# Kernel optimization log

Measured on AMD Instinct MI355X. Metric: run time of the kernel, lower is better.

The kernel has to match this reference:

```python
import jax, jax.numpy as jnp
import numpy as np

IN_C = 256
KEY_C = 256
VAL_C = 256
HEADS = 8


def setup_inputs() -> dict:
    key = jax.random.key(0)
    ks = jax.random.split(key, 9)
    s = 0.02
    return {
        "x": jax.random.normal(ks[0], (4, 8192, IN_C), dtype=jnp.float32),
        "Wk": jax.random.normal(ks[1], (KEY_C, IN_C), dtype=jnp.float32) * s,
        "bk": jax.random.normal(ks[2], (KEY_C,), dtype=jnp.float32) * s,
        "Wq": jax.random.normal(ks[3], (KEY_C, IN_C), dtype=jnp.float32) * s,
        "bq": jax.random.normal(ks[4], (KEY_C,), dtype=jnp.float32) * s,
        "Wv": jax.random.normal(ks[5], (VAL_C, IN_C), dtype=jnp.float32) * s,
        "bv": jax.random.normal(ks[6], (VAL_C,), dtype=jnp.float32) * s,
        "Wr": jax.random.normal(ks[7], (IN_C, VAL_C), dtype=jnp.float32) * s,
        "br": jax.random.normal(ks[8], (IN_C,), dtype=jnp.float32) * s,
    }


def reference(x, Wk, bk, Wq, bq, Wv, bv, Wr, br):
    n, N, c = x.shape
    # Faithful to torch: reshape (NOT transpose) of (n, N, c) into (n, c, N)
    xi = x.reshape(n, c, N)
    # 1x1 convs == channel-mixing matmuls over the token axis
    K = jnp.einsum('oc,ncs->nos', Wk, xi) + bk[None, :, None]
    Q = jnp.einsum('oc,ncs->nos', Wq, xi) + bq[None, :, None]
    V = jnp.einsum('oc,ncs->nos', Wv, xi) + bv[None, :, None]
    dk = KEY_C // HEADS
    dv = VAL_C // HEADS
    Kh = K.reshape(n, HEADS, dk, N)
    Qh = Q.reshape(n, HEADS, dk, N)
    Vh = V.reshape(n, HEADS, dv, N)
    # keys: softmax over tokens (dim=2); queries: softmax over head key channels (dim=1)
    Kh = jax.nn.softmax(Kh, axis=3)
    Qh = jax.nn.softmax(Qh, axis=2)
    # context = K @ V^T : [n, H, dk, dv]
    ctx = jnp.einsum('nhks,nhvs->nhkv', Kh, Vh)
    # attended = context^T @ Q : [n, H, dv, N]
    att = jnp.einsum('nhkv,nhks->nhvs', ctx, Qh)
    agg = att.reshape(n, VAL_C, N)
    rep = jnp.einsum('ov,nvs->nos', Wr, agg) + br[None, :, None]
    out = rep + xi  # residual in (n, c, N) layout
    return jnp.transpose(out, (0, 2, 1))  # (n, N, c)
```

## Files before the change

### kernel.cpp

```cpp
#include <hip/hip_runtime.h>

#define NTOK 8192
#define NCH  256
#define TT   64
#define XTP  264
#define EKP  72

typedef unsigned short u16;
typedef __attribute__((ext_vector_type(8))) short bf16x8;
typedef __attribute__((ext_vector_type(4))) float f32x4;
typedef __attribute__((ext_vector_type(8))) unsigned short u16x8;
typedef __attribute__((ext_vector_type(4))) unsigned short u16x4;

__device__ __forceinline__ float b2f(u16 h){
  union{unsigned u; float f;} x; x.u = ((unsigned)h) << 16; return x.f;
}
__device__ __forceinline__ u16 f2b(float f){
  union{float f; unsigned u;} x; x.f = f;
  unsigned u = x.u;
  return (u16)((u + 0x7FFFu + ((u >> 16) & 1u)) >> 16);
}
__device__ __forceinline__ f32x4 mfma16(bf16x8 a, bf16x8 b, f32x4 c){
  return __builtin_amdgcn_mfma_f32_16x16x32_bf16(a, b, c, 0, 0, 0);
}

__global__ __launch_bounds__(256)
void k_prep(const float* __restrict__ x,
            const float* __restrict__ Wk, const float* __restrict__ Wq,
            const float* __restrict__ Wv, const float* __restrict__ Wr,
            u16* __restrict__ xT, u16* __restrict__ wbf)
{
  __shared__ u16 ts[64 * 68];
  const int t = threadIdx.x, bid = blockIdx.x;
  if (bid < 2048) {
    const int b = bid >> 9, rem = bid & 511, tg = rem >> 2, cg = rem & 3;
    const float* xb = x + (size_t)b * NCH * NTOK;
    #pragma unroll
    for (int p = 0; p < 4; ++p) {
      int cl = p * 16 + (t >> 4);
      int tl = (t & 15) * 4;
      float4 v = *(const float4*)(xb + (size_t)(cg * 64 + cl) * NTOK + tg * 64 + tl);
      u16x4 pk; pk[0]=f2b(v.x); pk[1]=f2b(v.y); pk[2]=f2b(v.z); pk[3]=f2b(v.w);
      *(u16x4*)&ts[cl * 68 + tl] = pk;
    }
    __syncthreads();
    #pragma unroll
    for (int p = 0; p < 2; ++p) {
      int tl = p * 32 + (t >> 3);
      int cl = (t & 7) * 8;
      u16x8 o;
      #pragma unroll
      for (int j = 0; j < 8; ++j) o[j] = ts[(cl + j) * 68 + tl];
      *(u16x8*)(xT + (((size_t)(b * NTOK + tg * 64 + tl)) << 8) + cg * 64 + cl) = o;
    }
  } else {
    const int wb = bid - 2048;
    const int mat = wb >> 4;
    const float* src = (mat == 0) ? Wk : (mat == 1) ? Wq : (mat == 2) ? Wv : Wr;
    u16* dst = wbf + mat * 65536;
    const int base = (wb & 15) * 4096 + t * 16;
    #pragma unroll
    for (int i = 0; i < 4; ++i) {
      float4 v = *(const float4*)(src + base + i * 4);
      u16x4 pk; pk[0]=f2b(v.x); pk[1]=f2b(v.y); pk[2]=f2b(v.z); pk[3]=f2b(v.w);
      *(u16x4*)(dst + base + i * 4) = pk;
    }
  }
}

__global__ __launch_bounds__(512)
void k_ctx(const u16* __restrict__ xT, const u16* __restrict__ wbf,
           const float* __restrict__ bk, const float* __restrict__ bv,
           u16* __restrict__ ctxPart, float* __restrict__ denomPart)
{
  __shared__ u16 bufA[NCH * EKP];
  __shared__ u16 ekb[NCH * EKP];

  const int t = threadIdx.x;
  const int b = blockIdx.x >> 7, g = blockIdx.x & 127;
  const int w = t >> 6, lane = t & 63;
  const int l15 = lane & 15, quad = lane >> 4;
  const u16* Wkb = wbf;
  const u16* Wvb = wbf + 2 * 65536;

  {
    const u16* src = xT + ((size_t)(b * NTOK + g * TT) << 8);
    #pragma unroll
    for (int i = 0; i < 4; ++i) {
      int f = i * 4096 + t * 8;
      int tok = f >> 8, ch = f & 255;
      *(u16x8*)&bufA[tok * XTP + ch] = *(const u16x8*)(src + f);
    }
  }
  __syncthreads();

  f32x4 acc[2][4];

  #pragma unroll
  for (int mi = 0; mi < 2; ++mi)
    #pragma unroll
    for (int nj = 0; nj < 4; ++nj) acc[mi][nj] = (f32x4)0.f;
  for (int k0 = 0; k0 < NCH; k0 += 32) {
    bf16x8 af[2], bx[4];
    #pragma unroll
    for (int mi = 0; mi < 2; ++mi)
      af[mi] = *(const bf16x8*)(Wkb + (size_t)(w * 32 + mi * 16 + l15) * NCH + k0 + quad * 8);
    #pragma unroll
    for (int nj = 0; nj < 4; ++nj)
      bx[nj] = *(const bf16x8*)&bufA[(nj * 16 + l15) * XTP + k0 + quad * 8];
    #pragma unroll
    for (int mi = 0; mi < 2; ++mi)
      #pragma unroll
      for (int nj = 0; nj < 4; ++nj) acc[mi][nj] = mfma16(af[mi], bx[nj], acc[mi][nj]);
  }
  #pragma unroll
  for (int mi = 0; mi < 2; ++mi) {
    float4 bb = *(const float4*)(bk + w * 32 + mi * 16 + quad * 4);
    #pragma unroll
    for (int nj = 0; nj < 4; ++nj) {
      int tok = nj * 16 + l15, chb = w * 32 + mi * 16 + quad * 4;
      ekb[(chb + 0) * EKP + tok] = f2b(__expf(acc[mi][nj][0] + bb.x));
      ekb[(chb + 1) * EKP + tok] = f2b(__expf(acc[mi][nj][1] + bb.y));
      ekb[(chb + 2) * EKP + tok] = f2b(__expf(acc[mi][nj][2] + bb.z));
      ekb[(chb + 3) * EKP + tok] = f2b(__expf(acc[mi][nj][3] + bb.w));
    }
  }

  #pragma unroll
  for (int mi = 0; mi < 2; ++mi)
    #pragma unroll
    for (int nj = 0; nj < 4; ++nj) acc[mi][nj] = (f32x4)0.f;
  for (int k0 = 0; k0 < NCH; k0 += 32) {
    bf16x8 af[2], bx[4];
    #pragma unroll
    for (int mi = 0; mi < 2; ++mi)
      af[mi] = *(const bf16x8*)(Wvb + (size_t)(w * 32 + mi * 16 + l15) * NCH + k0 + quad * 8);
    #pragma unroll
    for (int nj = 0; nj < 4; ++nj)
      bx[nj] = *(const bf16x8*)&bufA[(nj * 16 + l15) * XTP + k0 + quad * 8];
    #pragma unroll
    for (int mi = 0; mi < 2; ++mi)
      #pragma unroll
      for (int nj = 0; nj < 4; ++nj) acc[mi][nj] = mfma16(af[mi], bx[nj], acc[mi][nj]);
  }
  __syncthreads();
  #pragma unroll
  for (int mi = 0; mi < 2; ++mi) {
    float4 bb = *(const float4*)(bv + w * 32 + mi * 16 + quad * 4);
    #pragma unroll
    for (int nj = 0; nj < 4; ++nj) {
      int tok = nj * 16 + l15, chb = w * 32 + mi * 16 + quad * 4;
      bufA[(chb + 0) * EKP + tok] = f2b(acc[mi][nj][0] + bb.x);
      bufA[(chb + 1) * EKP + tok] = f2b(acc[mi][nj][1] + bb.y);
      bufA[(chb + 2) * EKP + tok] = f2b(acc[mi][nj][2] + bb.z);
      bufA[(chb + 3) * EKP + tok] = f2b(acc[mi][nj][3] + bb.w);
    }
  }
  __syncthreads();

  f32x4 cacc[2][2];
  #pragma unroll
  for (int mi = 0; mi < 2; ++mi)
    #pragma unroll
    for (int nj = 0; nj < 2; ++nj) cacc[mi][nj] = (f32x4)0.f;
  #pragma unroll
  for (int kc = 0; kc < 2; ++kc) {
    bf16x8 ae[2], bvv[2];
    #pragma unroll
    for (int mi = 0; mi < 2; ++mi)
      ae[mi] = *(const bf16x8*)&ekb[(w * 32 + mi * 16 + l15) * EKP + kc * 32 + quad * 8];
    #pragma unroll
    for (int nj = 0; nj < 2; ++nj)
      bvv[nj] = *(const bf16x8*)&bufA[(w * 32 + nj * 16 + l15) * EKP + kc * 32 + quad * 8];
    #pragma unroll
    for (int mi = 0; mi < 2; ++mi)
      #pragma unroll
      for (int nj = 0; nj < 2; ++nj)
        cacc[mi][nj] = mfma16(ae[mi], bvv[nj], cacc[mi][nj]);
  }
  float dsum = 0.f;
  if (t < 256) {
    #pragma unroll
    for (int s = 0; s < TT; s += 8) {
      u16x8 v = *(const u16x8*)&ekb[t * EKP + s];
      #pragma unroll
      for (int j = 0; j < 8; ++j) dsum += b2f(v[j]);
    }
  }

  u16* cp = ctxPart + ((size_t)(b * 128 + g) << 13);
  #pragma unroll
  for (int mi = 0; mi < 2; ++mi)
    #pragma unroll
    for (int nj = 0; nj < 2; ++nj)
      #pragma unroll
      for (int r = 0; r < 4; ++r) {
        int e = ((w * 32 + mi * 16 + quad * 4 + r) << 5) + nj * 16 + l15;
        cp[e] = f2b(cacc[mi][nj][r]);
      }
  if (t < 256)
    denomPart[(size_t)(b * 128 + g) * 256 + t] = dsum;
}

__global__ __launch_bounds__(256)
void k_red(const u16* __restrict__ ctxPart, const float* __restrict__ denomPart,
           u16* __restrict__ ctxT, float* __restrict__ rdenomF)
{
  int i = blockIdx.x * 256 + threadIdx.x;
  if (i < 32768) {
    int b = i >> 13, e = i & 8191;
    const u16* p = ctxPart + ((size_t)(b * 128) << 13) + e;
    float s = 0.f;
    for (int g = 0; g < 128; ++g) s += b2f(p[(size_t)g << 13]);
    int hh = e >> 10, kk = (e >> 5) & 31, vch = e & 31;
    ctxT[(((b * 8 + hh) * 32 + vch) << 5) + kk] = f2b(s);
  } else if (i < 33792) {
    int j = i - 32768, b = j >> 8, ch = j & 255;
    const float* p = denomPart + (size_t)(b * 128) * 256 + ch;
    float s = 0.f;
    for (int g = 0; g < 128; ++g) s += p[(size_t)g << 8];
    rdenomF[j] = 1.0f / s;
  }
}

__global__ __launch_bounds__(512)
void k_out(const u16* __restrict__ xT, const u16* __restrict__ wbf,
           const float* __restrict__ bq, const float* __restrict__ br,
           const u16* __restrict__ ctxT, const float* __restrict__ rdenomF,
           float* __restrict__ out)
{
  __shared__ u16 xs[TT * XTP];
  __shared__ u16 qs[TT * XTP];

  const int t = threadIdx.x;
  const int b = blockIdx.x >> 7, g = blockIdx.x & 127;
  const int w = t >> 6, lane = t & 63;
  const int l15 = lane & 15, quad = lane >> 4;
  const u16* Wqb = wbf + 65536;
  const u16* Wrb = wbf + 3 * 65536;

  {
    const u16* src = xT + ((size_t)(b * NTOK + g * TT) << 8);
    #pragma unroll
    for (int i = 0; i < 4; ++i) {
      int f = i * 4096 + t * 8;
      int tok = f >> 8, ch = f & 255;
      *(u16x8*)&xs[tok * XTP + ch] = *(const u16x8*)(src + f);
    }
  }
  __syncthreads();

  f32x4 acc[2][4];
  #pragma unroll
  for (int mi = 0; mi < 2; ++mi)
    #pragma unroll
    for (int nj = 0; nj < 4; ++nj) acc[mi][nj] = (f32x4)0.f;
  for (int k0 = 0; k0 < NCH; k0 += 32) {
    bf16x8 af[2], bx[4];
    #pragma unroll
    for (int mi = 0; mi < 2; ++mi)
      af[mi] = *(const bf16x8*)(Wqb + (size_t)(w * 32 + mi * 16 + l15) * NCH + k0 + quad * 8);
    #pragma unroll
    for (int nj = 0; nj < 4; ++nj)
      bx[nj] = *(const bf16x8*)&xs[(nj * 16 + l15) * XTP + k0 + quad * 8];
    #pragma unroll
    for (int mi = 0; mi < 2; ++mi)
      #pragma unroll
      for (int nj = 0; nj < 4; ++nj) acc[mi][nj] = mfma16(af[mi], bx[nj], acc[mi][nj]);
  }
  #pragma unroll
  for (int mi = 0; mi < 2; ++mi) {
    float4 bb = *(const float4*)(bq + w * 32 + mi * 16 + quad * 4);
    #pragma unroll
    for (int nj = 0; nj < 4; ++nj) {
      acc[mi][nj][0] = __expf(acc[mi][nj][0] + bb.x);
      acc[mi][nj][1] = __expf(acc[mi][nj][1] + bb.y);
      acc[mi][nj][2] = __expf(acc[mi][nj][2] + bb.z);
      acc[mi][nj][3] = __expf(acc[mi][nj][3] + bb.w);
    }
  }
  float inv[4];
  #pragma unroll
  for (int nj = 0; nj < 4; ++nj) {
    float s = 0.f;
    #pragma unroll
    for (int mi = 0; mi < 2; ++mi)
      #pragma unroll
      for (int r = 0; r < 4; ++r) s += acc[mi][nj][r];
    s += __shfl_xor(s, 16);
    s += __shfl_xor(s, 32);
    inv[nj] = 1.0f / s;
  }
  #pragma unroll
  for (int mi = 0; mi < 2; ++mi) {
    float4 rd = *(const float4*)(rdenomF + b * 256 + w * 32 + mi * 16 + quad * 4);
    #pragma unroll
    for (int nj = 0; nj < 4; ++nj) {
      u16x4 pk;
      pk[0] = f2b(acc[mi][nj][0] * inv[nj] * rd.x);
      pk[1] = f2b(acc[mi][nj][1] * inv[nj] * rd.y);
      pk[2] = f2b(acc[mi][nj][2] * inv[nj] * rd.z);
      pk[3] = f2b(acc[mi][nj][3] * inv[nj] * rd.w);
      *(u16x4*)&qs[(nj * 16 + l15) * XTP + w * 32 + mi * 16 + quad * 4] = pk;
    }
  }
  __syncthreads();

  f32x4 aacc[2][4];
  {
    bf16x8 ac[2];
    #pragma unroll
    for (int mi = 0; mi < 2; ++mi)
      ac[mi] = *(const bf16x8*)(ctxT + (((size_t)(b * 8 + w) * 32 + mi * 16 + l15) << 5) + quad * 8);
    #pragma unroll
    for (int nj = 0; nj < 4; ++nj) {
      bf16x8 bqf = *(const bf16x8*)&qs[(nj * 16 + l15) * XTP + w * 32 + quad * 8];
      #pragma unroll
      for (int mi = 0; mi < 2; ++mi)
        aacc[mi][nj] = mfma16(ac[mi], bqf, (f32x4)0.f);
    }
  }
  #pragma unroll
  for (int mi = 0; mi < 2; ++mi)
    #pragma unroll
    for (int nj = 0; nj < 4; ++nj) {
      u16x4 pk;
      pk[0] = f2b(aacc[mi][nj][0]);
      pk[1] = f2b(aacc[mi][nj][1]);
      pk[2] = f2b(aacc[mi][nj][2]);
      pk[3] = f2b(aacc[mi][nj][3]);
      *(u16x4*)&qs[(nj * 16 + l15) * XTP + w * 32 + mi * 16 + quad * 4] = pk;
    }
  __syncthreads();

  #pragma unroll
  for (int mi = 0; mi < 2; ++mi)
    #pragma unroll
    for (int nj = 0; nj < 4; ++nj) acc[mi][nj] = (f32x4)0.f;
  for (int k0 = 0; k0 < NCH; k0 += 32) {
    bf16x8 af[2], bx[4];
    #pragma unroll
    for (int mi = 0; mi < 2; ++mi)
      af[mi] = *(const bf16x8*)(Wrb + (size_t)(w * 32 + mi * 16 + l15) * NCH + k0 + quad * 8);
    #pragma unroll
    for (int nj = 0; nj < 4; ++nj)
      bx[nj] = *(const bf16x8*)&qs[(nj * 16 + l15) * XTP + k0 + quad * 8];
    #pragma unroll
    for (int mi = 0; mi < 2; ++mi)
      #pragma unroll
      for (int nj = 0; nj < 4; ++nj) acc[mi][nj] = mfma16(af[mi], bx[nj], acc[mi][nj]);
  }
  #pragma unroll
  for (int mi = 0; mi < 2; ++mi) {
    float4 bb = *(const float4*)(br + w * 32 + mi * 16 + quad * 4);
    #pragma unroll
    for (int nj = 0; nj < 4; ++nj) {
      int tok = nj * 16 + l15;
      u16x4 rx = *(const u16x4*)&xs[tok * XTP + w * 32 + mi * 16 + quad * 4];
      float4 o;
      o.x = acc[mi][nj][0] + bb.x + b2f(rx[0]);
      o.y = acc[mi][nj][1] + bb.y + b2f(rx[1]);
      o.z = acc[mi][nj][2] + bb.z + b2f(rx[2]);
      o.w = acc[mi][nj][3] + bb.w + b2f(rx[3]);
      *(float4*)(out + (((size_t)(b * NTOK + g * TT + tok)) << 8) + w * 32 + mi * 16 + quad * 4) = o;
    }
  }
}

extern "C" void kernel_launch(void* const* d_in, const int* in_sizes, int n_in,
                              void* d_out, int out_size, void* d_ws, size_t ws_size,
                              hipStream_t stream) {
  const float* x  = (const float*)d_in[0];
  const float* Wk = (const float*)d_in[1];
  const float* bk = (const float*)d_in[2];
  const float* Wq = (const float*)d_in[3];
  const float* bq = (const float*)d_in[4];
  const float* Wv = (const float*)d_in[5];
  const float* bv = (const float*)d_in[6];
  const float* Wr = (const float*)d_in[7];
  const float* br = (const float*)d_in[8];
  float* out = (float*)d_out;

  char* wsb = (char*)d_ws;
  u16*   ctxPart   = (u16*)wsb;
  float* denomPart = (float*)(wsb + 8388608);
  u16*   ctxT      = (u16*)(wsb + 8912896);
  float* rdenomF   = (float*)(wsb + 8978432);
  u16*   wbf       = (u16*)(wsb + 8982528);
  u16*   xT        = (u16*)(wsb + 9506816);

  hipLaunchKernelGGL(k_prep, dim3(2112), dim3(256), 0, stream,
                     x, Wk, Wq, Wv, Wr, xT, wbf);
  hipLaunchKernelGGL(k_ctx, dim3(512), dim3(512), 0, stream,
                     xT, wbf, bk, bv, ctxPart, denomPart);
  hipLaunchKernelGGL(k_red, dim3(132), dim3(256), 0, stream,
                     ctxPart, denomPart, ctxT, rdenomF);
  hipLaunchKernelGGL(k_out, dim3(512), dim3(512), 0, stream,
                     xT, wbf, bq, br, ctxT, rdenomF, out);
}
```

Before: 148.5 us.

## Fuse prep, context, reduction and output kernels into one cooperative grid-synced kernel

Replaces the four launches with a single cooperative kernel of 256 blocks that each handle two token tiles, separated by grid.sync barriers. The x transpose and bf16 conversion now happen in shared memory inside the fused kernel, and the bf16 x tile is stored for reuse in the output phase. Weight fragments are held in registers across the k loop, and the partial reduction runs over 64 parts instead of 128. This removes launch gaps and some global round trips, at the cost of grid-wide syncs and only 256 blocks, which may leave compute units underused.

```diff
diff --git a/kernel.cpp b/kernel.cpp
--- a/kernel.cpp
+++ b/kernel.cpp
@@ -1,10 +1,14 @@
 #include <hip/hip_runtime.h>
+#include <hip/hip_cooperative_groups.h>
+
+namespace cg = cooperative_groups;
 
 #define NTOK 8192
 #define NCH  256
 #define TT   64
 #define XTP  264
 #define EKP  72
+#define TAP  70
 
 typedef unsigned short u16;
 typedef __attribute__((ext_vector_type(8))) short bf16x8;
@@ -23,347 +27,370 @@
 __device__ __forceinline__ f32x4 mfma16(bf16x8 a, bf16x8 b, f32x4 c){
   return __builtin_amdgcn_mfma_f32_16x16x32_bf16(a, b, c, 0, 0, 0);
 }
-
-__global__ __launch_bounds__(256)
-void k_prep(const float* __restrict__ x,
-            const float* __restrict__ Wk, const float* __restrict__ Wq,
-            const float* __restrict__ Wv, const float* __restrict__ Wr,
-            u16* __restrict__ xT, u16* __restrict__ wbf)
+__device__ __forceinline__ void load_wfrags(const u16* __restrict__ Wb, int row,
+                                            int quad, bf16x8* wf){
+  const u16* p = Wb + (size_t)row * NCH + quad * 8;
+  #pragma unroll
+  for (int k = 0; k < 8; ++k) wf[k] = *(const bf16x8*)(p + k * 32);
+}
+
+__global__ __launch_bounds__(512, 4)
+void k_fused(const float* __restrict__ x,
+             const float* __restrict__ Wk, const float* __restrict__ Wq,
+             const float* __restrict__ Wv, const float* __restrict__ Wr,
+             const float* __restrict__ bk, const float* __restrict__ bq,
+             const float* __restrict__ bv, const float* __restrict__ br,
+             u16* __restrict__ wbf, u16* __restrict__ xT,
+             u16* __restrict__ ctxPart, float* __restrict__ denomPart,
+             u16* __restrict__ ctxT, float* __restrict__ rdenomF,
+             float* __restrict__ out)
 {
-  __shared__ u16 ts[64 * 68];
-  const int t = threadIdx.x, bid = blockIdx.x;
-  if (bid < 2048) {
-    const int b = bid >> 9, rem = bid & 511, tg = rem >> 2, cg = rem & 3;
-    const float* xb = x + (size_t)b * NCH * NTOK;
-    #pragma unroll
-    for (int p = 0; p < 4; ++p) {
-      int cl = p * 16 + (t >> 4);
-      int tl = (t & 15) * 4;
-      float4 v = *(const float4*)(xb + (size_t)(cg * 64 + cl) * NTOK + tg * 64 + tl);
-      u16x4 pk; pk[0]=f2b(v.x); pk[1]=f2b(v.y); pk[2]=f2b(v.z); pk[3]=f2b(v.w);
-      *(u16x4*)&ts[cl * 68 + tl] = pk;
-    }
-    __syncthreads();
-    #pragma unroll
-    for (int p = 0; p < 2; ++p) {
-      int tl = p * 32 + (t >> 3);
-      int cl = (t & 7) * 8;
-      u16x8 o;
-      #pragma unroll
-      for (int j = 0; j < 8; ++j) o[j] = ts[(cl + j) * 68 + tl];
-      *(u16x8*)(xT + (((size_t)(b * NTOK + tg * 64 + tl)) << 8) + cg * 64 + cl) = o;
-    }
-  } else {
-    const int wb = bid - 2048;
-    const int mat = wb >> 4;
+  __shared__ u16 reg1[NCH * EKP];
+  __shared__ u16 reg2[NCH * EKP];
+
+  cg::grid_group grid = cg::this_grid();
+
+  const int t = threadIdx.x;
+  const int bid = blockIdx.x;
+  const int b = bid >> 6;
+  const int g0 = (bid & 63) * 2;
+  const int w = t >> 6, lane = t & 63;
+  const int l15 = lane & 15, quad = lane >> 4;
+  const int tok_t = t & 63, chb = (t >> 6) * 32;
+
+  if (bid < 64) {
+    const int mat = bid >> 4;
     const float* src = (mat == 0) ? Wk : (mat == 1) ? Wq : (mat == 2) ? Wv : Wr;
     u16* dst = wbf + mat * 65536;
-    const int base = (wb & 15) * 4096 + t * 16;
-    #pragma unroll
-    for (int i = 0; i < 4; ++i) {
+    const int base = (bid & 15) * 4096 + t * 8;
+    #pragma unroll
+    for (int i = 0; i < 2; ++i) {
       float4 v = *(const float4*)(src + base + i * 4);
       u16x4 pk; pk[0]=f2b(v.x); pk[1]=f2b(v.y); pk[2]=f2b(v.z); pk[3]=f2b(v.w);
       *(u16x4*)(dst + base + i * 4) = pk;
     }
-  }
-}
-
-__global__ __launch_bounds__(512)
-void k_ctx(const u16* __restrict__ xT, const u16* __restrict__ wbf,
-           const float* __restrict__ bk, const float* __restrict__ bv,
-           u16* __restrict__ ctxPart, float* __restrict__ denomPart)
-{
-  __shared__ u16 bufA[NCH * EKP];
-  __shared__ u16 ekb[NCH * EKP];
-
-  const int t = threadIdx.x;
-  const int b = blockIdx.x >> 7, g = blockIdx.x & 127;
-  const int w = t >> 6, lane = t & 63;
-  const int l15 = lane & 15, quad = lane >> 4;
-  const u16* Wkb = wbf;
-  const u16* Wvb = wbf + 2 * 65536;
+    __threadfence();
+  }
 
   {
-    const u16* src = xT + ((size_t)(b * NTOK + g * TT) << 8);
-    #pragma unroll
-    for (int i = 0; i < 4; ++i) {
-      int f = i * 4096 + t * 8;
-      int tok = f >> 8, ch = f & 255;
-      *(u16x8*)&bufA[tok * XTP + ch] = *(const u16x8*)(src + f);
-    }
-  }
-  __syncthreads();
-
-  f32x4 acc[2][4];
-
-  #pragma unroll
-  for (int mi = 0; mi < 2; ++mi)
-    #pragma unroll
-    for (int nj = 0; nj < 4; ++nj) acc[mi][nj] = (f32x4)0.f;
-  for (int k0 = 0; k0 < NCH; k0 += 32) {
-    bf16x8 af[2], bx[4];
-    #pragma unroll
-    for (int mi = 0; mi < 2; ++mi)
-      af[mi] = *(const bf16x8*)(Wkb + (size_t)(w * 32 + mi * 16 + l15) * NCH + k0 + quad * 8);
-    #pragma unroll
-    for (int nj = 0; nj < 4; ++nj)
-      bx[nj] = *(const bf16x8*)&bufA[(nj * 16 + l15) * XTP + k0 + quad * 8];
-    #pragma unroll
-    for (int mi = 0; mi < 2; ++mi)
-      #pragma unroll
-      for (int nj = 0; nj < 4; ++nj) acc[mi][nj] = mfma16(af[mi], bx[nj], acc[mi][nj]);
-  }
-  #pragma unroll
-  for (int mi = 0; mi < 2; ++mi) {
-    float4 bb = *(const float4*)(bk + w * 32 + mi * 16 + quad * 4);
-    #pragma unroll
-    for (int nj = 0; nj < 4; ++nj) {
-      int tok = nj * 16 + l15, chb = w * 32 + mi * 16 + quad * 4;
-      ekb[(chb + 0) * EKP + tok] = f2b(__expf(acc[mi][nj][0] + bb.x));
-      ekb[(chb + 1) * EKP + tok] = f2b(__expf(acc[mi][nj][1] + bb.y));
-      ekb[(chb + 2) * EKP + tok] = f2b(__expf(acc[mi][nj][2] + bb.z));
-      ekb[(chb + 3) * EKP + tok] = f2b(__expf(acc[mi][nj][3] + bb.w));
-    }
-  }
-
-  #pragma unroll
-  for (int mi = 0; mi < 2; ++mi)
-    #pragma unroll
-    for (int nj = 0; nj < 4; ++nj) acc[mi][nj] = (f32x4)0.f;
-  for (int k0 = 0; k0 < NCH; k0 += 32) {
-    bf16x8 af[2], bx[4];
-    #pragma unroll
-    for (int mi = 0; mi < 2; ++mi)
-      af[mi] = *(const bf16x8*)(Wvb + (size_t)(w * 32 + mi * 16 + l15) * NCH + k0 + quad * 8);
-    #pragma unroll
-    for (int nj = 0; nj < 4; ++nj)
-      bx[nj] = *(const bf16x8*)&bufA[(nj * 16 + l15) * XTP + k0 + quad * 8];
-    #pragma unroll
-    for (int mi = 0; mi < 2; ++mi)
-      #pragma unroll
-      for (int nj = 0; nj < 4; ++nj) acc[mi][nj] = mfma16(af[mi], bx[nj], acc[mi][nj]);
+    const float* xb = x + ((size_t)b * NCH) * NTOK + g0 * TT;
+    const int tq = (t & 15) * 4, ch0 = t >> 4;
+    #pragma unroll
+    for (int p = 0; p < 8; ++p) {
+      int ch = p * 32 + ch0;
+      float4 v = *(const float4*)(xb + (size_t)ch * NTOK + tq);
+      u16x4 pk; pk[0]=f2b(v.x); pk[1]=f2b(v.y); pk[2]=f2b(v.z); pk[3]=f2b(v.w);
+      *(u16x4*)&reg2[ch * TAP + tq] = pk;
+    }
   }
   __syncthreads();
   #pragma unroll
-  for (int mi = 0; mi < 2; ++mi) {
-    float4 bb = *(const float4*)(bv + w * 32 + mi * 16 + quad * 4);
-    #pragma unroll
-    for (int nj = 0; nj < 4; ++nj) {
-      int tok = nj * 16 + l15, chb = w * 32 + mi * 16 + quad * 4;
-      bufA[(chb + 0) * EKP + tok] = f2b(acc[mi][nj][0] + bb.x);
-      bufA[(chb + 1) * EKP + tok] = f2b(acc[mi][nj][1] + bb.y);
-      bufA[(chb + 2) * EKP + tok] = f2b(acc[mi][nj][2] + bb.z);
-      bufA[(chb + 3) * EKP + tok] = f2b(acc[mi][nj][3] + bb.w);
-    }
-  }
-  __syncthreads();
+  for (int i = 0; i < 4; ++i) {
+    u16x8 v;
+    #pragma unroll
+    for (int j = 0; j < 8; ++j) v[j] = reg2[(chb + i * 8 + j) * TAP + tok_t];
+    *(u16x8*)&reg1[tok_t * XTP + chb + i * 8] = v;
+  }
+  grid.sync();
+
+  const u16* Wkb = wbf;
+  const u16* Wqb = wbf + 65536;
+  const u16* Wvb = wbf + 2 * 65536;
+  const u16* Wrb = wbf + 3 * 65536;
 
   f32x4 cacc[2][2];
   #pragma unroll
   for (int mi = 0; mi < 2; ++mi)
     #pragma unroll
     for (int nj = 0; nj < 2; ++nj) cacc[mi][nj] = (f32x4)0.f;
-  #pragma unroll
-  for (int kc = 0; kc < 2; ++kc) {
-    bf16x8 ae[2], bvv[2];
+  float dsum = 0.f;
+
+  for (int c = 0; c < 2; ++c) {
+    if (c == 1) {
+      const float* xb = x + ((size_t)b * NCH) * NTOK + (g0 + 1) * TT;
+      const int tq = (t & 15) * 4, ch0 = t >> 4;
+      #pragma unroll
+      for (int p = 0; p < 8; ++p) {
+        int ch = p * 32 + ch0;
+        float4 v = *(const float4*)(xb + (size_t)ch * NTOK + tq);
+        u16x4 pk; pk[0]=f2b(v.x); pk[1]=f2b(v.y); pk[2]=f2b(v.z); pk[3]=f2b(v.w);
+        *(u16x4*)&reg2[ch * TAP + tq] = pk;
+      }
+      __syncthreads();
+      #pragma unroll
+      for (int i = 0; i < 4; ++i) {
+        u16x8 v;
+        #pragma unroll
+        for (int j = 0; j < 8; ++j) v[j] = reg2[(chb + i * 8 + j) * TAP + tok_t];
+        *(u16x8*)&reg1[tok_t * XTP + chb + i * 8] = v;
+      }
+      __syncthreads();
+    }
+
+    bf16x8 wfA[8], wfB[8];
+    load_wfrags(Wkb, w * 32 + l15, quad, wfA);
+
+    {
+      u16* dst = xT + ((size_t)(bid * 2 + c)) * 16384;
+      #pragma unroll
+      for (int i = 0; i < 4; ++i) {
+        int f = i * 4096 + t * 8;
+        *(u16x8*)(dst + f) = *(const u16x8*)&reg1[(f >> 8) * XTP + (f & 255)];
+      }
+    }
+
+    const u16* abase = &reg1[l15 * XTP + quad * 8];
+    f32x4 acc0[4], acc1[4];
+
+    load_wfrags(Wkb, w * 32 + 16 + l15, quad, wfB);
+    #pragma unroll
+    for (int mi = 0; mi < 4; ++mi) acc0[mi] = (f32x4)0.f;
+    #pragma unroll
+    for (int k = 0; k < 8; ++k) {
+      #pragma unroll
+      for (int mi = 0; mi < 4; ++mi) {
+        bf16x8 a = *(const bf16x8*)(abase + mi * 16 * XTP + k * 32);
+        acc0[mi] = mfma16(a, wfA[k], acc0[mi]);
+      }
+    }
+    {
+      float bb = bk[w * 32 + l15];
+      #pragma unroll
+      for (int mi = 0; mi < 4; ++mi) {
+        u16x4 pk;
+        #pragma unroll
+        for (int r = 0; r < 4; ++r) pk[r] = f2b(__expf(acc0[mi][r] + bb));
+        *(u16x4*)&reg2[(w * 32 + l15) * EKP + mi * 16 + quad * 4] = pk;
+      }
+    }
+    load_wfrags(Wvb, w * 32 + l15, quad, wfA);
+    #pragma unroll
+    for (int mi = 0; mi < 4; ++mi) acc0[mi] = (f32x4)0.f;
+    #pragma unroll
+    for (int k = 0; k < 8; ++k) {
+      #pragma unroll
+      for (int mi = 0; mi < 4; ++mi) {
+        bf16x8 a = *(const bf16x8*)(abase + mi * 16 * XTP + k * 32);
+        acc0[mi] = mfma16(a, wfB[k], acc0[mi]);
+      }
+    }
+    {
+      float bb = bk[w * 32 + 16 + l15];
+      #pragma unroll
+      for (int mi = 0; mi < 4; ++mi) {
+        u16x4 pk;
+        #pragma unroll
+        for (int r = 0; r < 4; ++r) pk[r] = f2b(__expf(acc0[mi][r] + bb));
+        *(u16x4*)&reg2[(w * 32 + 16 + l15) * EKP + mi * 16 + quad * 4] = pk;
+      }
+    }
+    load_wfrags(Wvb, w * 32 + 16 + l15, quad, wfB);
+    #pragma unroll
+    for (int mi = 0; mi < 4; ++mi) { acc0[mi] = (f32x4)0.f; acc1[mi] = (f32x4)0.f; }
+    #pragma unroll
+    for (int k = 0; k < 8; ++k) {
+      #pragma unroll
+      for (int mi = 0; mi < 4; ++mi) {
+        bf16x8 a = *(const bf16x8*)(abase + mi * 16 * XTP + k * 32);
+        acc0[mi] = mfma16(a, wfA[k], acc0[mi]);
+        acc1[mi] = mfma16(a, wfB[k], acc1[mi]);
+      }
+    }
+    __syncthreads();
+    {
+      float b0 = bv[w * 32 + l15], b1 = bv[w * 32 + 16 + l15];
+      #pragma unroll
+      for (int mi = 0; mi < 4; ++mi) {
+        u16x4 p0, p1;
+        #pragma unroll
+        for (int r = 0; r < 4; ++r) { p0[r] = f2b(acc0[mi][r] + b0); p1[r] = f2b(acc1[mi][r] + b1); }
+        *(u16x4*)&reg1[(w * 32 + l15) * EKP + mi * 16 + quad * 4] = p0;
+        *(u16x4*)&reg1[(w * 32 + 16 + l15) * EKP + mi * 16 + quad * 4] = p1;
+      }
+    }
+    #pragma unroll
+    for (int kc = 0; kc < 2; ++kc) {
+      bf16x8 ae[2], bvv[2];
+      #pragma unroll
+      for (int mi = 0; mi < 2; ++mi)
+        ae[mi] = *(const bf16x8*)&reg2[(w * 32 + mi * 16 + l15) * EKP + kc * 32 + quad * 8];
+      #pragma unroll
+      for (int nj = 0; nj < 2; ++nj)
+        bvv[nj] = *(const bf16x8*)&reg1[(w * 32 + nj * 16 + l15) * EKP + kc * 32 + quad * 8];
+      #pragma unroll
+      for (int mi = 0; mi < 2; ++mi)
+        #pragma unroll
+        for (int nj = 0; nj < 2; ++nj)
+          cacc[mi][nj] = mfma16(ae[mi], bvv[nj], cacc[mi][nj]);
+    }
+    if (t < 256) {
+      #pragma unroll
+      for (int s = 0; s < TT; s += 8) {
+        u16x8 v = *(const u16x8*)&reg2[t * EKP + s];
+        #pragma unroll
+        for (int j = 0; j < 8; ++j) dsum += b2f(v[j]);
+      }
+    }
+    __syncthreads();
+  }
+
+  {
+    u16* cp = ctxPart + ((size_t)bid << 13);
     #pragma unroll
     for (int mi = 0; mi < 2; ++mi)
-      ae[mi] = *(const bf16x8*)&ekb[(w * 32 + mi * 16 + l15) * EKP + kc * 32 + quad * 8];
-    #pragma unroll
-    for (int nj = 0; nj < 2; ++nj)
-      bvv[nj] = *(const bf16x8*)&bufA[(w * 32 + nj * 16 + l15) * EKP + kc * 32 + quad * 8];
+      #pragma unroll
+      for (int nj = 0; nj < 2; ++nj)
+        #pragma unroll
+        for (int r = 0; r < 4; ++r) {
+          int e = ((w * 32 + mi * 16 + quad * 4 + r) << 5) + nj * 16 + l15;
+          cp[e] = f2b(cacc[mi][nj][r]);
+        }
+    if (t < 256)
+      denomPart[(size_t)bid * 256 + t] = dsum;
+  }
+  __threadfence();
+  grid.sync();
+
+  if (bid < 66) {
+    int i = bid * 512 + t;
+    if (i < 32768) {
+      int bb_ = i >> 13, e = i & 8191;
+      const u16* p = ctxPart + ((size_t)(bb_ * 64) << 13) + e;
+      float s = 0.f;
+      for (int gg = 0; gg < 64; ++gg) s += b2f(p[(size_t)gg << 13]);
+      int hh = e >> 10, kk = (e >> 5) & 31, vch = e & 31;
+      ctxT[(((bb_ * 8 + hh) * 32 + vch) << 5) + kk] = f2b(s);
+    } else if (i < 33792) {
+      int j = i - 32768, bb_ = j >> 8, ch = j & 255;
+      const float* p = denomPart + (size_t)(bb_ * 64) * 256 + ch;
+      float s = 0.f;
+      for (int gg = 0; gg < 64; ++gg) s += p[(size_t)gg << 8];
+      rdenomF[j] = 1.0f / s;
+    }
+    __threadfence();
+  }
+  grid.sync();
+
+  for (int c = 0; c < 2; ++c) {
+    const int s0 = (g0 + c) * TT;
+
+    {
+      const u16* src = xT + ((size_t)(bid * 2 + c)) * 16384;
+      #pragma unroll
+      for (int i = 0; i < 4; ++i) {
+        int f = i * 4096 + t * 8;
+        *(u16x8*)&reg1[(f >> 8) * XTP + (f & 255)] = *(const u16x8*)(src + f);
+      }
+    }
+    bf16x8 wfA[8], wfB[8];
+    load_wfrags(Wqb, w * 32 + l15, quad, wfA);
+    load_wfrags(Wqb, w * 32 + 16 + l15, quad, wfB);
+    __syncthreads();
+
+    f32x4 qa[2][4];
+    #pragma unroll
+    for (int nj = 0; nj < 4; ++nj) { qa[0][nj] = (f32x4)0.f; qa[1][nj] = (f32x4)0.f; }
+    #pragma unroll
+    for (int k = 0; k < 8; ++k) {
+      #pragma unroll
+      for (int nj = 0; nj < 4; ++nj) {
+        bf16x8 bx = *(const bf16x8*)&reg1[(nj * 16 + l15) * XTP + k * 32 + quad * 8];
+        qa[0][nj] = mfma16(wfA[k], bx, qa[0][nj]);
+        qa[1][nj] = mfma16(wfB[k], bx, qa[1][nj]);
+      }
+    }
+    #pragma unroll
+    for (int mi = 0; mi < 2; ++mi) {
+      float4 bb = *(const float4*)(bq + w * 32 + mi * 16 + quad * 4);
+      #pragma unroll
+      for (int nj = 0; nj < 4; ++nj) {
+        qa[mi][nj][0] = __expf(qa[mi][nj][0] + bb.x);
+        qa[mi][nj][1] = __expf(qa[mi][nj][1] + bb.y);
+        qa[mi][nj][2] = __expf(qa[mi][nj][2] + bb.z);
+        qa[mi][nj][3] = __expf(qa[mi][nj][3] + bb.w);
+      }
+    }
+    float inv[4];
+    #pragma unroll
+    for (int nj = 0; nj < 4; ++nj) {
+      float s = 0.f;
+      #pragma unroll
+      for (int mi = 0; mi < 2; ++mi)
+        #pragma unroll
+        for (int r = 0; r < 4; ++r) s += qa[mi][nj][r];
+      s += __shfl_xor(s, 16);
+      s += __shfl_xor(s, 32);
+      inv[nj] = 1.0f / s;
+    }
+    #pragma unroll
+    for (int mi = 0; mi < 2; ++mi) {
+      float4 rd = *(const float4*)(rdenomF + b * 256 + w * 32 + mi * 16 + quad * 4);
+      #pragma unroll
+      for (int nj = 0; nj < 4; ++nj) {
+        u16x4 pk;
+        pk[0] = f2b(qa[mi][nj][0] * inv[nj] * rd.x);
+        pk[1] = f2b(qa[mi][nj][1] * inv[nj] * rd.y);
+        pk[2] = f2b(qa[mi][nj][2] * inv[nj] * rd.z);
+        pk[3] = f2b(qa[mi][nj][3] * inv[nj] * rd.w);
+        *(u16x4*)&reg2[(nj * 16 + l15) * XTP + w * 32 + mi * 16 + quad * 4] = pk;
+      }
+    }
+    __syncthreads();
+
+    f32x4 aacc[2][4];
+    {
+      bf16x8 ac[2];
+      #pragma unroll
+      for (int mi = 0; mi < 2; ++mi)
+        ac[mi] = *(const bf16x8*)(ctxT + (((size_t)(b * 8 + w) * 32 + mi * 16 + l15) << 5) + quad * 8);
+      #pragma unroll
+      for (int nj = 0; nj < 4; ++nj) {
+        bf16x8 bqf = *(const bf16x8*)&reg2[(nj * 16 + l15) * XTP + w * 32 + quad * 8];
+        #pragma unroll
+        for (int mi = 0; mi < 2; ++mi)
+          aacc[mi][nj] = mfma16(ac[mi], bqf, (f32x4)0.f);
+      }
+    }
+    load_wfrags(Wrb, w * 32 + l15, quad, wfA);
     #pragma unroll
     for (int mi = 0; mi < 2; ++mi)
       #pragma unroll
-      for (int nj = 0; nj < 2; ++nj)
-        cacc[mi][nj] = mfma16(ae[mi], bvv[nj], cacc[mi][nj]);
-  }
-  float dsum = 0.f;
-  if (t < 256) {
-    #pragma unroll
-    for (int s = 0; s < TT; s += 8) {
-      u16x8 v = *(const u16x8*)&ekb[t * EKP + s];
-      #pragma unroll
-      for (int j = 0; j < 8; ++j) dsum += b2f(v[j]);
-    }
-  }
-
-  u16* cp = ctxPart + ((size_t)(b * 128 + g) << 13);
-  #pragma unroll
-  for (int mi = 0; mi < 2; ++mi)
-    #pragma unroll
-    for (int nj = 0; nj < 2; ++nj)
-      #pragma unroll
-      for (int r = 0; r < 4; ++r) {
-        int e = ((w * 32 + mi * 16 + quad * 4 + r) << 5) + nj * 16 + l15;
-        cp[e] = f2b(cacc[mi][nj][r]);
-      }
-  if (t < 256)
-    denomPart[(size_t)(b * 128 + g) * 256 + t] = dsum;
-}
-
-__global__ __launch_bounds__(256)
-void k_red(const u16* __restrict__ ctxPart, const float* __restrict__ denomPart,
-           u16* __restrict__ ctxT, float* __restrict__ rdenomF)
-{
-  int i = blockIdx.x * 256 + threadIdx.x;
-  if (i < 32768) {
-    int b = i >> 13, e = i & 8191;
-    const u16* p = ctxPart + ((size_t)(b * 128) << 13) + e;
-    float s = 0.f;
-    for (int g = 0; g < 128; ++g) s += b2f(p[(size_t)g << 13]);
-    int hh = e >> 10, kk = (e >> 5) & 31, vch = e & 31;
-    ctxT[(((b * 8 + hh) * 32 + vch) << 5) + kk] = f2b(s);
-  } else if (i < 33792) {
-    int j = i - 32768, b = j >> 8, ch = j & 255;
-    const float* p = denomPart + (size_t)(b * 128) * 256 + ch;
-    float s = 0.f;
-    for (int g = 0; g < 128; ++g) s += p[(size_t)g << 8];
-    rdenomF[j] = 1.0f / s;
-  }
-}
-
-__global__ __launch_bounds__(512)
-void k_out(const u16* __restrict__ xT, const u16* __restrict__ wbf,
-           const float* __restrict__ bq, const float* __restrict__ br,
-           const u16* __restrict__ ctxT, const float* __restrict__ rdenomF,
-           float* __restrict__ out)
-{
-  __shared__ u16 xs[TT * XTP];
-  __shared__ u16 qs[TT * XTP];
-
-  const int t = threadIdx.x;
-  const int b = blockIdx.x >> 7, g = blockIdx.x & 127;
-  const int w = t >> 6, lane = t & 63;
-  const int l15 = lane & 15, quad = lane >> 4;
-  const u16* Wqb = wbf + 65536;
-  const u16* Wrb = wbf + 3 * 65536;
-
-  {
-    const u16* src = xT + ((size_t)(b * NTOK + g * TT) << 8);
-    #pragma unroll
-    for (int i = 0; i < 4; ++i) {
-      int f = i * 4096 + t * 8;
-      int tok = f >> 8, ch = f & 255;
-      *(u16x8*)&xs[tok * XTP + ch] = *(const u16x8*)(src + f);
-    }
-  }
-  __syncthreads();
-
-  f32x4 acc[2][4];
-  #pragma unroll
-  for (int mi = 0; mi < 2; ++mi)
-    #pragma unroll
-    for (int nj = 0; nj < 4; ++nj) acc[mi][nj] = (f32x4)0.f;
-  for (int k0 = 0; k0 < NCH; k0 += 32) {
-    bf16x8 af[2], bx[4];
-    #pragma unroll
-    for (int mi = 0; mi < 2; ++mi)
-      af[mi] = *(const bf16x8*)(Wqb + (size_t)(w * 32 + mi * 16 + l15) * NCH + k0 + quad * 8);
-    #pragma unroll
-    for (int nj = 0; nj < 4; ++nj)
-      bx[nj] = *(const bf16x8*)&xs[(nj * 16 + l15) * XTP + k0 + quad * 8];
-    #pragma unroll
-    for (int mi = 0; mi < 2; ++mi)
-      #pragma unroll
-      for (int nj = 0; nj < 4; ++nj) acc[mi][nj] = mfma16(af[mi], bx[nj], acc[mi][nj]);
-  }
-  #pragma unroll
-  for (int mi = 0; mi < 2; ++mi) {
-    float4 bb = *(const float4*)(bq + w * 32 + mi * 16 + quad * 4);
-    #pragma unroll
-    for (int nj = 0; nj < 4; ++nj) {
-      acc[mi][nj][0] = __expf(acc[mi][nj][0] + bb.x);
-      acc[mi][nj][1] = __expf(acc[mi][nj][1] + bb.y);
-      acc[mi][nj][2] = __expf(acc[mi][nj][2] + bb.z);
-      acc[mi][nj][3] = __expf(acc[mi][nj][3] + bb.w);
-    }
-  }
-  float inv[4];
-  #pragma unroll
-  for (int nj = 0; nj < 4; ++nj) {
-    float s = 0.f;
-    #pragma unroll
-    for (int mi = 0; mi < 2; ++mi)
-      #pragma unroll
-      for (int r = 0; r < 4; ++r) s += acc[mi][nj][r];
-    s += __shfl_xor(s, 16);
-    s += __shfl_xor(s, 32);
-    inv[nj] = 1.0f / s;
-  }
-  #pragma unroll
-  for (int mi = 0; mi < 2; ++mi) {
-    float4 rd = *(const float4*)(rdenomF + b * 256 + w * 32 + mi * 16 + quad * 4);
-    #pragma unroll
-    for (int nj = 0; nj < 4; ++nj) {
-      u16x4 pk;
-      pk[0] = f2b(acc[mi][nj][0] * inv[nj] * rd.x);
-      pk[1] = f2b(acc[mi][nj][1] * inv[nj] * rd.y);
-      pk[2] = f2b(acc[mi][nj][2] * inv[nj] * rd.z);
-      pk[3] = f2b(acc[mi][nj][3] * inv[nj] * rd.w);
-      *(u16x4*)&qs[(nj * 16 + l15) * XTP + w * 32 + mi * 16 + quad * 4] = pk;
-    }
-  }
-  __syncthreads();
-
-  f32x4 aacc[2][4];
-  {
-    bf16x8 ac[2];
-    #pragma unroll
-    for (int mi = 0; mi < 2; ++mi)
-      ac[mi] = *(const bf16x8*)(ctxT + (((size_t)(b * 8 + w) * 32 + mi * 16 + l15) << 5) + quad * 8);
-    #pragma unroll
-    for (int nj = 0; nj < 4; ++nj) {
-      bf16x8 bqf = *(const bf16x8*)&qs[(nj * 16 + l15) * XTP + w * 32 + quad * 8];
-      #pragma unroll
-      for (int mi = 0; mi < 2; ++mi)
-        aacc[mi][nj] = mfma16(ac[mi], bqf, (f32x4)0.f);
-    }
-  }
-  #pragma unroll
-  for (int mi = 0; mi < 2; ++mi)
-    #pragma unroll
-    for (int nj = 0; nj < 4; ++nj) {
-      u16x4 pk;
-      pk[0] = f2b(aacc[mi][nj][0]);
-      pk[1] = f2b(aacc[mi][nj][1]);
-      pk[2] = f2b(aacc[mi][nj][2]);
-      pk[3] = f2b(aacc[mi][nj][3]);
-      *(u16x4*)&qs[(nj * 16 + l15) * XTP + w * 32 + mi * 16 + quad * 4] = pk;
-    }
-  __syncthreads();
-
-  #pragma unroll
-  for (int mi = 0; mi < 2; ++mi)
-    #pragma unroll
-    for (int nj = 0; nj < 4; ++nj) acc[mi][nj] = (f32x4)0.f;
-  for (int k0 = 0; k0 < NCH; k0 += 32) {
-    bf16x8 af[2], bx[4];
-    #pragma unroll
-    for (int mi = 0; mi < 2; ++mi)
-      af[mi] = *(const bf16x8*)(Wrb + (size_t)(w * 32 + mi * 16 + l15) * NCH + k0 + quad * 8);
-    #pragma unroll
-    for (int nj = 0; nj < 4; ++nj)
-      bx[nj] = *(const bf16x8*)&qs[(nj * 16 + l15) * XTP + k0 + quad * 8];
-    #pragma unroll
-    for (int mi = 0; mi < 2; ++mi)
-      #pragma unroll
-      for (int nj = 0; nj < 4; ++nj) acc[mi][nj] = mfma16(af[mi], bx[nj], acc[mi][nj]);
-  }
-  #pragma unroll
-  for (int mi = 0; mi < 2; ++mi) {
-    float4 bb = *(const float4*)(br + w * 32 + mi * 16 + quad * 4);
-    #pragma unroll
-    for (int nj = 0; nj < 4; ++nj) {
-      int tok = nj * 16 + l15;
-      u16x4 rx = *(const u16x4*)&xs[tok * XTP + w * 32 + mi * 16 + quad * 4];
-      float4 o;
-      o.x = acc[mi][nj][0] + bb.x + b2f(rx[0]);
-      o.y = acc[mi][nj][1] + bb.y + b2f(rx[1]);
-      o.z = acc[mi][nj][2] + bb.z + b2f(rx[2]);
-      o.w = acc[mi][nj][3] + bb.w + b2f(rx[3]);
-      *(float4*)(out + (((size_t)(b * NTOK + g * TT + tok)) << 8) + w * 32 + mi * 16 + quad * 4) = o;
-    }
+      for (int nj = 0; nj < 4; ++nj) {
+        u16x4 pk;
+        pk[0] = f2b(aacc[mi][nj][0]); pk[1] = f2b(aacc[mi][nj][1]);
+        pk[2] = f2b(aacc[mi][nj][2]); pk[3] = f2b(aacc[mi][nj][3]);
+        *(u16x4*)&reg2[(nj * 16 + l15) * XTP + w * 32 + mi * 16 + quad * 4] = pk;
+      }
+    __syncthreads();
+
+    load_wfrags(Wrb, w * 32 + 16 + l15, quad, wfB);
+    #pragma unroll
+    for (int nj = 0; nj < 4; ++nj) { qa[0][nj] = (f32x4)0.f; qa[1][nj] = (f32x4)0.f; }
+    #pragma unroll
+    for (int k = 0; k < 8; ++k) {
+      #pragma unroll
+      for (int nj = 0; nj < 4; ++nj) {
+        bf16x8 bx = *(const bf16x8*)&reg2[(nj * 16 + l15) * XTP + k * 32 + quad * 8];
+        qa[0][nj] = mfma16(wfA[k], bx, qa[0][nj]);
+        qa[1][nj] = mfma16(wfB[k], bx, qa[1][nj]);
+      }
+    }
+    #pragma unroll
+    for (int mi = 0; mi < 2; ++mi) {
+      float4 bb = *(const float4*)(br + w * 32 + mi * 16 + quad * 4);
+      #pragma unroll
+      for (int nj = 0; nj < 4; ++nj) {
+        int tok = nj * 16 + l15;
+        u16x4 rx = *(const u16x4*)&reg1[tok * XTP + w * 32 + mi * 16 + quad * 4];
+        float4 o;
+        o.x = qa[mi][nj][0] + bb.x + b2f(rx[0]);
+        o.y = qa[mi][nj][1] + bb.y + b2f(rx[1]);
+        o.z = qa[mi][nj][2] + bb.z + b2f(rx[2]);
+        o.w = qa[mi][nj][3] + bb.w + b2f(rx[3]);
+        *(float4*)(out + (((size_t)(b * NTOK + s0 + tok)) << 8) + w * 32 + mi * 16 + quad * 4) = o;
+      }
+    }
+    __syncthreads();
   }
 }
 
@@ -383,18 +410,15 @@
 
   char* wsb = (char*)d_ws;
   u16*   ctxPart   = (u16*)wsb;
-  float* denomPart = (float*)(wsb + 8388608);
-  u16*   ctxT      = (u16*)(wsb + 8912896);
-  float* rdenomF   = (float*)(wsb + 8978432);
-  u16*   wbf       = (u16*)(wsb + 8982528);
-  u16*   xT        = (u16*)(wsb + 9506816);
-
-  hipLaunchKernelGGL(k_prep, dim3(2112), dim3(256), 0, stream,
-                     x, Wk, Wq, Wv, Wr, xT, wbf);
-  hipLaunchKernelGGL(k_ctx, dim3(512), dim3(512), 0, stream,
-                     xT, wbf, bk, bv, ctxPart, denomPart);
-  hipLaunchKernelGGL(k_red, dim3(132), dim3(256), 0, stream,
-                     ctxPart, denomPart, ctxT, rdenomF);
-  hipLaunchKernelGGL(k_out, dim3(512), dim3(512), 0, stream,
-                     xT, wbf, bq, br, ctxT, rdenomF, out);
-}
+  float* denomPart = (float*)(wsb + 4194304);
+  u16*   ctxT      = (u16*)(wsb + 4456448);
+  float* rdenomF   = (float*)(wsb + 4521984);
+  u16*   wbf       = (u16*)(wsb + 4526080);
+  u16*   xT        = (u16*)(wsb + 5050368);
+
+  void* args[] = {(void*)&x, (void*)&Wk, (void*)&Wq, (void*)&Wv, (void*)&Wr,
+                  (void*)&bk, (void*)&bq, (void*)&bv, (void*)&br,
+                  (void*)&wbf, (void*)&xT, (void*)&ctxPart, (void*)&denomPart,
+                  (void*)&ctxT, (void*)&rdenomF, (void*)&out};
+  hipLaunchCooperativeKernel((void*)k_fused, dim3(256), dim3(512), args, 0, stream);
+}
```

New measurement: 371.7 us. 150% more time.
